# Optimization experiments

Measured on AMD Instinct MI355X. Metric: run time of the kernel, lower is better.

Reference implementation:

```python
import jax, jax.numpy as jnp
import numpy as np

F0 = 39          # FIELD_COUNT
D = 16           # embedding dim
SIZES = [128, 128, 128]  # cross_layer_sizes
B = 8192


def setup_inputs() -> dict:
    key = jax.random.key(0)
    k0, k1, k2, k3, k4 = jax.random.split(key, 5)
    nn_input = jax.random.normal(k0, (B, F0 * D), dtype=jnp.float32)
    # direct=False => field_nums: [39, 64, 64]; filters: [F0*Fk, L]
    scale = 0.02
    f0 = jax.random.normal(k1, (F0 * F0, SIZES[0]), dtype=jnp.float32) * scale
    f1 = jax.random.normal(k2, (F0 * (SIZES[0] // 2), SIZES[1]), dtype=jnp.float32) * scale
    f2 = jax.random.normal(k3, (F0 * (SIZES[1] // 2), SIZES[2]), dtype=jnp.float32) * scale
    final_len = SIZES[0] // 2 + SIZES[1] // 2 + SIZES[2]  # 256
    w_nn = jax.random.normal(k4, (final_len, 1), dtype=jnp.float32) * scale
    b_nn = jnp.zeros((1,), dtype=jnp.float32)
    return {"nn_input": nn_input, "f0": f0, "f1": f1, "f2": f2,
            "w_nn": w_nn, "b_nn": b_nn}


def reference(nn_input, f0, f1, f2, w_nn, b_nn):
    x0 = nn_input.reshape(-1, F0, D)            # [B, F0, D]
    b = x0.shape[0]
    filters = [f0, f1, f2]
    hidden = x0
    field = F0
    direct_outs = []
    n_layers = len(SIZES)
    for idx, layer_size in enumerate(SIZES):
        # dim-wise outer product: z[b,d,i*field+j] = x0[b,i,d]*hidden[b,j,d]
        z = jnp.einsum('bid,bjd->bdij', x0, hidden).reshape(b, D, F0 * field)
        if idx == 0:
            # remove self-interactions: keep strictly upper triangle, x2
            mask = jnp.triu(jnp.ones((F0, F0), dtype=z.dtype), k=1).reshape(1, 1, F0 * F0)
            z = z * mask * 2.0
        # conv1d kernel-width-1 == per-position GEMM; fuse the [0,2,1] transpose
        curr = jnp.einsum('bdc,cl->bld', z, filters[idx])   # [B, L, D]
        curr = jax.nn.relu(curr)                            # cross_activation='relu'
        if idx != n_layers - 1:
            half = layer_size // 2
            next_hidden = curr[:, :half, :]
            direct = curr[:, half:, :]
        else:
            direct = curr
            next_hidden = None
        direct_outs.append(direct)
        hidden = next_hidden
        field = layer_size // 2
    result = jnp.concatenate(direct_outs, axis=1)   # [B, final_len, D]
    rs = result.sum(axis=-1)                        # [B, final_len]
    base_score = rs.sum(axis=1, keepdims=True)      # res=True
    return base_score + rs @ w_nn + b_nn            # [B, 1]
```

## Files before the change

### kernel.cpp

```cpp
#include <hip/hip_runtime.h>


#define F0N 39
#define NB  32
#define NC16 156
#define LAYER_HALVES (NC16 * 4 * 64 * 8)

typedef _Float16 half8 __attribute__((ext_vector_type(8)));
typedef float f32x16 __attribute__((ext_vector_type(16)));

__global__ void prep_kernel(const float* __restrict__ f0,
                            const float* __restrict__ f1,
                            const float* __restrict__ f2,
                            _Float16* __restrict__ fprep) {
    int blk  = blockIdx.x;
    int l    = blk / NC16;
    int c16  = blk - l * NC16;
    int t    = threadIdx.x;
    int nt   = t >> 6;
    int lane = t & 63;
    int hf   = lane >> 5;
    int n    = nt * 32 + (lane & 31);
    const float* f = (l == 0) ? f0 : ((l == 1) ? f1 : f2);
    half8 v;
    #pragma unroll
    for (int reg = 0; reg < 8; ++reg) {
        int kg = c16 * 16 + hf * 8 + reg;
        float x;
        if (l == 0) {
            int fi = kg >> 6, fj = kg & 63;
            x = (fj < F0N) ? f[(fi * F0N + fj) * 128 + n] : 0.0f;
        } else {
            x = f[(size_t)kg * 128 + n];
        }
        v[reg] = (_Float16)x;
    }
    *(half8*)&fprep[(size_t)l * LAYER_HALVES + (((c16 * 4 + nt) * 64 + lane) << 3)] = v;
}

#define LOAD_BF(C16)                                                          \
    half8 Bf[4];                                                              \
    {                                                                         \
        _Pragma("unroll")                                                     \
        for (int nt = 0; nt < 4; ++nt)                                        \
            Bf[nt] = *(const half8*)(fpl + ((((C16) * 4 + nt) * 64 + lane) << 3)); \
    }

#define DO_MFMA()                                                             \
    {                                                                         \
        _Pragma("unroll")                                                     \
        for (int mt = 0; mt < 2; ++mt)                                        \
            _Pragma("unroll")                                                 \
            for (int nt = 0; nt < 4; ++nt)                                    \
                acc[mt][nt] = __builtin_amdgcn_mfma_f32_32x32x16_f16(         \
                    Af[mt], Bf[nt], acc[mt][nt], 0, 0, 0);                    \
    }

#define FULL_STEP(Q)                                                          \
    do {                                                                      \
        LOAD_BF(i * 4 + (Q));                                                 \
        half8 Af[2];                                                          \
        _Pragma("unroll")                                                     \
        for (int mt = 0; mt < 2; ++mt) Af[mt] = hreg[mt][(Q)] * xv2[mt];      \
        DO_MFMA();                                                            \
    } while (0)

#define PART_STEP(Q)                                                          \
    do {                                                                      \
        LOAD_BF(i * 4 + (Q));                                                 \
        const int j0 = (Q) * 16 + hf * 8;                                     \
        half8 msk;                                                            \
        _Pragma("unroll")                                                     \
        for (int reg = 0; reg < 8; ++reg)                                     \
            msk[reg] = (j0 + reg > i) ? (_Float16)1.0f : (_Float16)0.0f;      \
        half8 Af[2];                                                          \
        _Pragma("unroll")                                                     \
        for (int mt = 0; mt < 2; ++mt) Af[mt] = hreg[mt][(Q)] * (msk * xv2[mt]); \
        DO_MFMA();                                                            \
    } while (0)

__global__ __launch_bounds__(512, 2) void cin_mfma(
    const float* __restrict__ xin,
    const _Float16* __restrict__ fprep,
    const float* __restrict__ wnn,
    const float* __restrict__ bnn,
    float* __restrict__ out)
{
    __shared__ _Float16 hT[NB * 16 * 72] __attribute__((aligned(16)));
    __shared__ _Float16 xs[NB * 16 * 40] __attribute__((aligned(16)));
    __shared__ float outacc[NB];

    const int t     = threadIdx.x;
    const int wave  = t >> 6;
    const int lane  = t & 63;
    const int hf    = lane >> 5;
    const int lane5 = lane & 31;
    const int dl    = lane & 15;
    const int bt    = lane5 >> 4;
    const int wb0   = wave * 4;
    const int b0    = blockIdx.x * NB;

    for (int u = t; u < NB * 16 * 72 / 8; u += 512) ((uint4*)hT)[u] = uint4{0, 0, 0, 0};
    if (t < NB) outacc[t] = 0.0f;
    __syncthreads();

    for (int u = t; u < NB * F0N; u += 512) {
        int nb = u / F0N;
        int i  = u - nb * F0N;
        const float* src = xin + (size_t)(b0 + nb) * 624 + i * 16;
        #pragma unroll
        for (int q = 0; q < 4; ++q) {
            float4 v = *(const float4*)(src + q * 4);
            int d = q * 4;
            hT[(nb * 16 + d + 0) * 72 + i] = (_Float16)v.x;
            hT[(nb * 16 + d + 1) * 72 + i] = (_Float16)v.y;
            hT[(nb * 16 + d + 2) * 72 + i] = (_Float16)v.z;
            hT[(nb * 16 + d + 3) * 72 + i] = (_Float16)v.w;
            xs[(nb * 16 + d + 0) * 40 + i] = (_Float16)v.x;
            xs[(nb * 16 + d + 1) * 40 + i] = (_Float16)v.y;
            xs[(nb * 16 + d + 2) * 40 + i] = (_Float16)v.z;
            xs[(nb * 16 + d + 3) * 40 + i] = (_Float16)v.w;
        }
    }
    __syncthreads();

    for (int layer = 0; layer < 3; ++layer) {
        half8 hreg[2][4];
        #pragma unroll
        for (int mt = 0; mt < 2; ++mt) {
            int base = ((wb0 + mt * 2 + bt) * 16 + dl) * 72 + hf * 8;
            #pragma unroll
            for (int r = 0; r < 4; ++r)
                hreg[mt][r] = *(const half8*)&hT[base + r * 16];
        }
        __syncthreads();

        f32x16 acc[2][4];
        #pragma unroll
        for (int mt = 0; mt < 2; ++mt)
            #pragma unroll
            for (int nt = 0; nt < 4; ++nt)
                #pragma unroll
                for (int e = 0; e < 16; ++e) acc[mt][nt][e] = 0.0f;

        const _Float16* fpl = fprep + (size_t)layer * LAYER_HALVES;
        const int xrow0 = ((wb0 + bt) * 16 + dl) * 40;
        const int xrow1 = ((wb0 + 2 + bt) * 16 + dl) * 40;

        if (layer == 0) {
            _Float16 xv2[2];
            for (int i = 0; i < 16; ++i) {
                xv2[0] = (_Float16)2.0f * xs[xrow0 + i];
                xv2[1] = (_Float16)2.0f * xs[xrow1 + i];
                if (i < 15) PART_STEP(0);
                FULL_STEP(1);
                FULL_STEP(2);
            }
            for (int i = 16; i < 32; ++i) {
                xv2[0] = (_Float16)2.0f * xs[xrow0 + i];
                xv2[1] = (_Float16)2.0f * xs[xrow1 + i];
                if (i < 31) PART_STEP(1);
                FULL_STEP(2);
            }
            for (int i = 32; i < 38; ++i) {
                xv2[0] = (_Float16)2.0f * xs[xrow0 + i];
                xv2[1] = (_Float16)2.0f * xs[xrow1 + i];
                PART_STEP(2);
            }
        } else {
            _Float16 xv2[2];
            for (int i = 0; i < F0N; ++i) {
                xv2[0] = xs[xrow0 + i];
                xv2[1] = xs[xrow1 + i];
                FULL_STEP(0);
                FULL_STEP(1);
                FULL_STEP(2);
                FULL_STEP(3);
            }
        }

        const int catbase = (layer == 2) ? 128 : ((layer == 0) ? -64 : 0);
        #pragma unroll
        for (int mt = 0; mt < 2; ++mt) {
            const int nb0 = wb0 + mt * 2;
            float cm0 = 0.0f, cm1 = 0.0f;
            #pragma unroll
            for (int nt = 0; nt < 4; ++nt) {
                float r[16];
                #pragma unroll
                for (int reg = 0; reg < 16; ++reg)
                    r[reg] = fmaxf(acc[mt][nt][reg], 0.0f);
                if (layer < 2 && nt < 2) {
                    const int j = nt * 32 + lane5;
                    #pragma unroll
                    for (int reg = 0; reg < 16; ++reg) {
                        int nb = nb0 + (reg >> 3);
                        int d  = (reg & 3) + 8 * ((reg >> 2) & 1) + 4 * hf;
                        hT[(nb * 16 + d) * 72 + j] = (_Float16)r[reg];
                    }
                }
                if (layer == 2 || nt >= 2) {
                    const float w = 1.0f + wnn[catbase + nt * 32 + lane5];
                    float s0 = ((r[0] + r[1]) + (r[2] + r[3])) +
                               ((r[4] + r[5]) + (r[6] + r[7]));
                    float s1 = ((r[8] + r[9]) + (r[10] + r[11])) +
                               ((r[12] + r[13]) + (r[14] + r[15]));
                    s0 += __shfl_xor(s0, 32, 64);
                    s1 += __shfl_xor(s1, 32, 64);
                    cm0 = fmaf(s0, w, cm0);
                    cm1 = fmaf(s1, w, cm1);
                }
            }
            #pragma unroll
            for (int sh = 16; sh >= 1; sh >>= 1) {
                cm0 += __shfl_xor(cm0, sh, 64);
                cm1 += __shfl_xor(cm1, sh, 64);
            }
            if (lane == 0) {
                atomicAdd(&outacc[nb0], cm0);
                atomicAdd(&outacc[nb0 + 1], cm1);
            }
        }
        __syncthreads();
    }

    if (t < NB) out[b0 + t] = outacc[t] + bnn[0];
}

extern "C" void kernel_launch(void* const* d_in, const int* in_sizes, int n_in,
                              void* d_out, int out_size, void* d_ws, size_t ws_size,
                              hipStream_t stream) {
    const float* xin = (const float*)d_in[0];
    const float* f0g = (const float*)d_in[1];
    const float* f1g = (const float*)d_in[2];
    const float* f2g = (const float*)d_in[3];
    const float* wnn = (const float*)d_in[4];
    const float* bnn = (const float*)d_in[5];
    float* out = (float*)d_out;
    _Float16* fprep = (_Float16*)d_ws;

    prep_kernel<<<3 * NC16, 256, 0, stream>>>(f0g, f1g, f2g, fprep);

    const int B = in_sizes[0] / 624;
    cin_mfma<<<B / NB, 512, 0, stream>>>(xin, fprep, wnn, bnn, out);
}
```

Before: 255.6 us.

## Fold triangular mask into prepped filters, shrink block to 8 samples per block

The strict upper-triangle mask and the factor of 2 for layer 0 are moved into the filter prep kernel, so the inner loop no longer builds per-step masks. Each wave now handles one M-tile of two samples instead of two, halving accumulator registers. Blocks go from 512 to 256 threads over 8 samples, giving 4x more blocks and higher occupancy. The x values are stored pre-duplicated as packed half2 words so they can be splatted cheaply. The tradeoff is that each B-fragment load from global memory now feeds half as many MFMAs, which doubles filter traffic per sample.

```diff
diff --git a/kernel.cpp b/kernel.cpp
--- a/kernel.cpp
+++ b/kernel.cpp
@@ -2,9 +2,10 @@
 
 
 #define F0N 39
-#define NB  32
+#define NB  8
 #define NC16 156
 #define LAYER_HALVES (NC16 * 4 * 64 * 8)
+#define XW 41
 
 typedef _Float16 half8 __attribute__((ext_vector_type(8)));
 typedef float f32x16 __attribute__((ext_vector_type(16)));
@@ -29,7 +30,7 @@
         float x;
         if (l == 0) {
             int fi = kg >> 6, fj = kg & 63;
-            x = (fj < F0N) ? f[(fi * F0N + fj) * 128 + n] : 0.0f;
+            x = (fj < F0N && fj > fi) ? 2.0f * f[(fi * F0N + fj) * 128 + n] : 0.0f;
         } else {
             x = f[(size_t)kg * 128 + n];
         }
@@ -46,40 +47,23 @@
             Bf[nt] = *(const half8*)(fpl + ((((C16) * 4 + nt) * 64 + lane) << 3)); \
     }
 
-#define DO_MFMA()                                                             \
-    {                                                                         \
-        _Pragma("unroll")                                                     \
-        for (int mt = 0; mt < 2; ++mt)                                        \
-            _Pragma("unroll")                                                 \
-            for (int nt = 0; nt < 4; ++nt)                                    \
-                acc[mt][nt] = __builtin_amdgcn_mfma_f32_32x32x16_f16(         \
-                    Af[mt], Bf[nt], acc[mt][nt], 0, 0, 0);                    \
-    }
+static __device__ inline half8 splat8(unsigned xw) {
+    union { unsigned u[4]; half8 h; } s;
+    s.u[0] = xw; s.u[1] = xw; s.u[2] = xw; s.u[3] = xw;
+    return s.h;
+}
 
 #define FULL_STEP(Q)                                                          \
     do {                                                                      \
         LOAD_BF(i * 4 + (Q));                                                 \
-        half8 Af[2];                                                          \
+        half8 Af = hreg[(Q)] * splat8(xw);                                    \
         _Pragma("unroll")                                                     \
-        for (int mt = 0; mt < 2; ++mt) Af[mt] = hreg[mt][(Q)] * xv2[mt];      \
-        DO_MFMA();                                                            \
+        for (int nt = 0; nt < 4; ++nt)                                        \
+            acc[nt] = __builtin_amdgcn_mfma_f32_32x32x16_f16(                 \
+                Af, Bf[nt], acc[nt], 0, 0, 0);                                \
     } while (0)
 
-#define PART_STEP(Q)                                                          \
-    do {                                                                      \
-        LOAD_BF(i * 4 + (Q));                                                 \
-        const int j0 = (Q) * 16 + hf * 8;                                     \
-        half8 msk;                                                            \
-        _Pragma("unroll")                                                     \
-        for (int reg = 0; reg < 8; ++reg)                                     \
-            msk[reg] = (j0 + reg > i) ? (_Float16)1.0f : (_Float16)0.0f;      \
-        half8 Af[2];                                                          \
-        _Pragma("unroll")                                                     \
-        for (int mt = 0; mt < 2; ++mt) Af[mt] = hreg[mt][(Q)] * (msk * xv2[mt]); \
-        DO_MFMA();                                                            \
-    } while (0)
-
-__global__ __launch_bounds__(512, 2) void cin_mfma(
+__global__ __launch_bounds__(256, 4) void cin_mfma(
     const float* __restrict__ xin,
     const _Float16* __restrict__ fprep,
     const float* __restrict__ wnn,
@@ -87,7 +71,7 @@
     float* __restrict__ out)
 {
     __shared__ _Float16 hT[NB * 16 * 72] __attribute__((aligned(16)));
-    __shared__ _Float16 xs[NB * 16 * 40] __attribute__((aligned(16)));
+    __shared__ unsigned  xs2[NB * 16 * XW] __attribute__((aligned(16)));
     __shared__ float outacc[NB];
 
     const int t     = threadIdx.x;
@@ -97,14 +81,14 @@
     const int lane5 = lane & 31;
     const int dl    = lane & 15;
     const int bt    = lane5 >> 4;
-    const int wb0   = wave * 4;
+    const int nbw   = wave * 2;
     const int b0    = blockIdx.x * NB;
 
-    for (int u = t; u < NB * 16 * 72 / 8; u += 512) ((uint4*)hT)[u] = uint4{0, 0, 0, 0};
+    for (int u = t; u < NB * 16 * 72 / 8; u += 256) ((uint4*)hT)[u] = uint4{0, 0, 0, 0};
     if (t < NB) outacc[t] = 0.0f;
     __syncthreads();
 
-    for (int u = t; u < NB * F0N; u += 512) {
+    for (int u = t; u < NB * F0N; u += 256) {
         int nb = u / F0N;
         int i  = u - nb * F0N;
         const float* src = xin + (size_t)(b0 + nb) * 624 + i * 16;
@@ -112,66 +96,57 @@
         for (int q = 0; q < 4; ++q) {
             float4 v = *(const float4*)(src + q * 4);
             int d = q * 4;
+            union { _Float16 f[2]; unsigned u; } pk;
             hT[(nb * 16 + d + 0) * 72 + i] = (_Float16)v.x;
             hT[(nb * 16 + d + 1) * 72 + i] = (_Float16)v.y;
             hT[(nb * 16 + d + 2) * 72 + i] = (_Float16)v.z;
             hT[(nb * 16 + d + 3) * 72 + i] = (_Float16)v.w;
-            xs[(nb * 16 + d + 0) * 40 + i] = (_Float16)v.x;
-            xs[(nb * 16 + d + 1) * 40 + i] = (_Float16)v.y;
-            xs[(nb * 16 + d + 2) * 40 + i] = (_Float16)v.z;
-            xs[(nb * 16 + d + 3) * 40 + i] = (_Float16)v.w;
+            pk.f[0] = pk.f[1] = (_Float16)v.x; xs2[(nb * 16 + d + 0) * XW + i] = pk.u;
+            pk.f[0] = pk.f[1] = (_Float16)v.y; xs2[(nb * 16 + d + 1) * XW + i] = pk.u;
+            pk.f[0] = pk.f[1] = (_Float16)v.z; xs2[(nb * 16 + d + 2) * XW + i] = pk.u;
+            pk.f[0] = pk.f[1] = (_Float16)v.w; xs2[(nb * 16 + d + 3) * XW + i] = pk.u;
         }
     }
     __syncthreads();
 
     for (int layer = 0; layer < 3; ++layer) {
-        half8 hreg[2][4];
-        #pragma unroll
-        for (int mt = 0; mt < 2; ++mt) {
-            int base = ((wb0 + mt * 2 + bt) * 16 + dl) * 72 + hf * 8;
+        half8 hreg[4];
+        {
+            int base = ((nbw + bt) * 16 + dl) * 72 + hf * 8;
             #pragma unroll
             for (int r = 0; r < 4; ++r)
-                hreg[mt][r] = *(const half8*)&hT[base + r * 16];
+                hreg[r] = *(const half8*)&hT[base + r * 16];
         }
         __syncthreads();
 
-        f32x16 acc[2][4];
-        #pragma unroll
-        for (int mt = 0; mt < 2; ++mt)
+        f32x16 acc[4];
+        #pragma unroll
+        for (int nt = 0; nt < 4; ++nt)
             #pragma unroll
-            for (int nt = 0; nt < 4; ++nt)
-                #pragma unroll
-                for (int e = 0; e < 16; ++e) acc[mt][nt][e] = 0.0f;
+            for (int e = 0; e < 16; ++e) acc[nt][e] = 0.0f;
 
         const _Float16* fpl = fprep + (size_t)layer * LAYER_HALVES;
-        const int xrow0 = ((wb0 + bt) * 16 + dl) * 40;
-        const int xrow1 = ((wb0 + 2 + bt) * 16 + dl) * 40;
+        const int xrow = ((nbw + bt) * 16 + dl) * XW;
 
         if (layer == 0) {
-            _Float16 xv2[2];
             for (int i = 0; i < 16; ++i) {
-                xv2[0] = (_Float16)2.0f * xs[xrow0 + i];
-                xv2[1] = (_Float16)2.0f * xs[xrow1 + i];
-                if (i < 15) PART_STEP(0);
+                const unsigned xw = xs2[xrow + i];
+                if (i < 15) FULL_STEP(0);
                 FULL_STEP(1);
                 FULL_STEP(2);
             }
             for (int i = 16; i < 32; ++i) {
-                xv2[0] = (_Float16)2.0f * xs[xrow0 + i];
-                xv2[1] = (_Float16)2.0f * xs[xrow1 + i];
-                if (i < 31) PART_STEP(1);
+                const unsigned xw = xs2[xrow + i];
+                if (i < 31) FULL_STEP(1);
                 FULL_STEP(2);
             }
             for (int i = 32; i < 38; ++i) {
-                xv2[0] = (_Float16)2.0f * xs[xrow0 + i];
-                xv2[1] = (_Float16)2.0f * xs[xrow1 + i];
-                PART_STEP(2);
+                const unsigned xw = xs2[xrow + i];
+                FULL_STEP(2);
             }
         } else {
-            _Float16 xv2[2];
             for (int i = 0; i < F0N; ++i) {
-                xv2[0] = xs[xrow0 + i];
-                xv2[1] = xs[xrow1 + i];
+                const unsigned xw = xs2[xrow + i];
                 FULL_STEP(0);
                 FULL_STEP(1);
                 FULL_STEP(2);
@@ -180,46 +155,42 @@
         }
 
         const int catbase = (layer == 2) ? 128 : ((layer == 0) ? -64 : 0);
-        #pragma unroll
-        for (int mt = 0; mt < 2; ++mt) {
-            const int nb0 = wb0 + mt * 2;
-            float cm0 = 0.0f, cm1 = 0.0f;
+        float cm0 = 0.0f, cm1 = 0.0f;
+        #pragma unroll
+        for (int nt = 0; nt < 4; ++nt) {
+            float r[16];
             #pragma unroll
-            for (int nt = 0; nt < 4; ++nt) {
-                float r[16];
+            for (int reg = 0; reg < 16; ++reg)
+                r[reg] = fmaxf(acc[nt][reg], 0.0f);
+            if (layer < 2 && nt < 2) {
+                const int j = nt * 32 + lane5;
                 #pragma unroll
-                for (int reg = 0; reg < 16; ++reg)
-                    r[reg] = fmaxf(acc[mt][nt][reg], 0.0f);
-                if (layer < 2 && nt < 2) {
-                    const int j = nt * 32 + lane5;
-                    #pragma unroll
-                    for (int reg = 0; reg < 16; ++reg) {
-                        int nb = nb0 + (reg >> 3);
-                        int d  = (reg & 3) + 8 * ((reg >> 2) & 1) + 4 * hf;
-                        hT[(nb * 16 + d) * 72 + j] = (_Float16)r[reg];
-                    }
+                for (int reg = 0; reg < 16; ++reg) {
+                    int nb = nbw + (reg >> 3);
+                    int d  = (reg & 3) + 8 * ((reg >> 2) & 1) + 4 * hf;
+                    hT[(nb * 16 + d) * 72 + j] = (_Float16)r[reg];
                 }
-                if (layer == 2 || nt >= 2) {
-                    const float w = 1.0f + wnn[catbase + nt * 32 + lane5];
-                    float s0 = ((r[0] + r[1]) + (r[2] + r[3])) +
-                               ((r[4] + r[5]) + (r[6] + r[7]));
-                    float s1 = ((r[8] + r[9]) + (r[10] + r[11])) +
-                               ((r[12] + r[13]) + (r[14] + r[15]));
-                    s0 += __shfl_xor(s0, 32, 64);
-                    s1 += __shfl_xor(s1, 32, 64);
-                    cm0 = fmaf(s0, w, cm0);
-                    cm1 = fmaf(s1, w, cm1);
-                }
-            }
-            #pragma unroll
-            for (int sh = 16; sh >= 1; sh >>= 1) {
-                cm0 += __shfl_xor(cm0, sh, 64);
-                cm1 += __shfl_xor(cm1, sh, 64);
-            }
-            if (lane == 0) {
-                atomicAdd(&outacc[nb0], cm0);
-                atomicAdd(&outacc[nb0 + 1], cm1);
-            }
+            }
+            if (layer == 2 || nt >= 2) {
+                const float w = 1.0f + wnn[catbase + nt * 32 + lane5];
+                float s0 = ((r[0] + r[1]) + (r[2] + r[3])) +
+                           ((r[4] + r[5]) + (r[6] + r[7]));
+                float s1 = ((r[8] + r[9]) + (r[10] + r[11])) +
+                           ((r[12] + r[13]) + (r[14] + r[15]));
+                s0 += __shfl_xor(s0, 32, 64);
+                s1 += __shfl_xor(s1, 32, 64);
+                cm0 = fmaf(s0, w, cm0);
+                cm1 = fmaf(s1, w, cm1);
+            }
+        }
+        #pragma unroll
+        for (int sh = 16; sh >= 1; sh >>= 1) {
+            cm0 += __shfl_xor(cm0, sh, 64);
+            cm1 += __shfl_xor(cm1, sh, 64);
+        }
+        if (lane == 0) {
+            atomicAdd(&outacc[nbw], cm0);
+            atomicAdd(&outacc[nbw + 1], cm1);
         }
         __syncthreads();
     }
@@ -242,5 +213,5 @@
     prep_kernel<<<3 * NC16, 256, 0, stream>>>(f0g, f1g, f2g, fprep);
 
     const int B = in_sizes[0] / 624;
-    cin_mfma<<<B / NB, 512, 0, stream>>>(xin, fprep, wnn, bnn, out);
-}
+    cin_mfma<<<B / NB, 256, 0, stream>>>(xin, fprep, wnn, bnn, out);
+}
```

Measured after the change: 603.0 us. 2.36x slower.

## Stage filter tiles through double-buffered LDS and fold triangle mask into weights

Applied to the files above, without the earlier changes.

Filter fragments were previously loaded straight from global memory by every wave. Now the block cooperatively loads each per-i filter slice into a double-buffered shared-memory stage, prefetching the next slice while MFMAs run on the current one. The layer-0 upper-triangle mask and the factor of 2 are moved into the prepared filter weights, so the per-step mask construction goes away. The cost is 32 KB of extra LDS, which may reduce occupancy, plus a block-wide barrier on every iteration.

```diff
diff --git a/kernel.cpp b/kernel.cpp
--- a/kernel.cpp
+++ b/kernel.cpp
@@ -5,6 +5,7 @@
 #define NB  32
 #define NC16 156
 #define LAYER_HALVES (NC16 * 4 * 64 * 8)
+#define IHALFS 8192
 
 typedef _Float16 half8 __attribute__((ext_vector_type(8)));
 typedef float f32x16 __attribute__((ext_vector_type(16)));
@@ -29,7 +30,7 @@
         float x;
         if (l == 0) {
             int fi = kg >> 6, fj = kg & 63;
-            x = (fj < F0N) ? f[(fi * F0N + fj) * 128 + n] : 0.0f;
+            x = (fj < F0N && fj > fi) ? 2.0f * f[(fi * F0N + fj) * 128 + n] : 0.0f;
         } else {
             x = f[(size_t)kg * 128 + n];
         }
@@ -38,45 +39,34 @@
     *(half8*)&fprep[(size_t)l * LAYER_HALVES + (((c16 * 4 + nt) * 64 + lane) << 3)] = v;
 }
 
-#define LOAD_BF(C16)                                                          \
-    half8 Bf[4];                                                              \
-    {                                                                         \
+#define FULL_STEP_LS(Q)                                                       \
+    do {                                                                      \
+        half8 Bf[4];                                                          \
         _Pragma("unroll")                                                     \
         for (int nt = 0; nt < 4; ++nt)                                        \
-            Bf[nt] = *(const half8*)(fpl + ((((C16) * 4 + nt) * 64 + lane) << 3)); \
-    }
-
-#define DO_MFMA()                                                             \
-    {                                                                         \
+            Bf[nt] = *(const half8*)&bcur[(((Q) * 4 + nt) * 64 + lane) << 3]; \
+        half8 Af[2];                                                          \
+        _Pragma("unroll")                                                     \
+        for (int mt = 0; mt < 2; ++mt) Af[mt] = hreg[mt][(Q)] * xv2[mt];      \
         _Pragma("unroll")                                                     \
         for (int mt = 0; mt < 2; ++mt)                                        \
             _Pragma("unroll")                                                 \
             for (int nt = 0; nt < 4; ++nt)                                    \
                 acc[mt][nt] = __builtin_amdgcn_mfma_f32_32x32x16_f16(         \
                     Af[mt], Bf[nt], acc[mt][nt], 0, 0, 0);                    \
-    }
-
-#define FULL_STEP(Q)                                                          \
+    } while (0)
+
+#define STAGE_LOAD(IP)                                                        \
     do {                                                                      \
-        LOAD_BF(i * 4 + (Q));                                                 \
-        half8 Af[2];                                                          \
-        _Pragma("unroll")                                                     \
-        for (int mt = 0; mt < 2; ++mt) Af[mt] = hreg[mt][(Q)] * xv2[mt];      \
-        DO_MFMA();                                                            \
+        const uint4* g = (const uint4*)(fpl + (size_t)(IP) * IHALFS);         \
+        s0 = g[t];                                                            \
+        s1 = g[t + 512];                                                      \
     } while (0)
 
-#define PART_STEP(Q)                                                          \
+#define STAGE_WRITE(BUFP)                                                     \
     do {                                                                      \
-        LOAD_BF(i * 4 + (Q));                                                 \
-        const int j0 = (Q) * 16 + hf * 8;                                     \
-        half8 msk;                                                            \
-        _Pragma("unroll")                                                     \
-        for (int reg = 0; reg < 8; ++reg)                                     \
-            msk[reg] = (j0 + reg > i) ? (_Float16)1.0f : (_Float16)0.0f;      \
-        half8 Af[2];                                                          \
-        _Pragma("unroll")                                                     \
-        for (int mt = 0; mt < 2; ++mt) Af[mt] = hreg[mt][(Q)] * (msk * xv2[mt]); \
-        DO_MFMA();                                                            \
+        ((uint4*)(BUFP))[t]       = s0;                                       \
+        ((uint4*)(BUFP))[t + 512] = s1;                                       \
     } while (0)
 
 __global__ __launch_bounds__(512, 2) void cin_mfma(
@@ -88,6 +78,7 @@
 {
     __shared__ _Float16 hT[NB * 16 * 72] __attribute__((aligned(16)));
     __shared__ _Float16 xs[NB * 16 * 40] __attribute__((aligned(16)));
+    __shared__ _Float16 bst[2][IHALFS] __attribute__((aligned(16)));
     __shared__ float outacc[NB];
 
     const int t     = threadIdx.x;
@@ -125,6 +116,11 @@
     __syncthreads();
 
     for (int layer = 0; layer < 3; ++layer) {
+        const _Float16* fpl = fprep + (size_t)layer * LAYER_HALVES;
+        uint4 s0, s1;
+
+        STAGE_LOAD(0);
+
         half8 hreg[2][4];
         #pragma unroll
         for (int mt = 0; mt < 2; ++mt) {
@@ -133,6 +129,9 @@
             for (int r = 0; r < 4; ++r)
                 hreg[mt][r] = *(const half8*)&hT[base + r * 16];
         }
+        __syncthreads();
+
+        STAGE_WRITE(bst[0]);
         __syncthreads();
 
         f32x16 acc[2][4];
@@ -143,39 +142,37 @@
                 #pragma unroll
                 for (int e = 0; e < 16; ++e) acc[mt][nt][e] = 0.0f;
 
-        const _Float16* fpl = fprep + (size_t)layer * LAYER_HALVES;
         const int xrow0 = ((wb0 + bt) * 16 + dl) * 40;
         const int xrow1 = ((wb0 + 2 + bt) * 16 + dl) * 40;
 
         if (layer == 0) {
             _Float16 xv2[2];
-            for (int i = 0; i < 16; ++i) {
-                xv2[0] = (_Float16)2.0f * xs[xrow0 + i];
-                xv2[1] = (_Float16)2.0f * xs[xrow1 + i];
-                if (i < 15) PART_STEP(0);
-                FULL_STEP(1);
-                FULL_STEP(2);
-            }
-            for (int i = 16; i < 32; ++i) {
-                xv2[0] = (_Float16)2.0f * xs[xrow0 + i];
-                xv2[1] = (_Float16)2.0f * xs[xrow1 + i];
-                if (i < 31) PART_STEP(1);
-                FULL_STEP(2);
-            }
-            for (int i = 32; i < 38; ++i) {
-                xv2[0] = (_Float16)2.0f * xs[xrow0 + i];
-                xv2[1] = (_Float16)2.0f * xs[xrow1 + i];
-                PART_STEP(2);
+            for (int i = 0; i < 38; ++i) {
+                const _Float16* bcur = bst[i & 1];
+                _Float16* bnxt = bst[(i & 1) ^ 1];
+                if (i < 37) STAGE_LOAD(i + 1);
+                xv2[0] = xs[xrow0 + i];
+                xv2[1] = xs[xrow1 + i];
+                if (i < 15) FULL_STEP_LS(0);
+                if (i < 31) FULL_STEP_LS(1);
+                if (i < 37) STAGE_WRITE(bnxt);
+                FULL_STEP_LS(2);
+                __syncthreads();
             }
         } else {
             _Float16 xv2[2];
             for (int i = 0; i < F0N; ++i) {
+                const _Float16* bcur = bst[i & 1];
+                _Float16* bnxt = bst[(i & 1) ^ 1];
+                if (i < F0N - 1) STAGE_LOAD(i + 1);
                 xv2[0] = xs[xrow0 + i];
                 xv2[1] = xs[xrow1 + i];
-                FULL_STEP(0);
-                FULL_STEP(1);
-                FULL_STEP(2);
-                FULL_STEP(3);
+                FULL_STEP_LS(0);
+                FULL_STEP_LS(1);
+                FULL_STEP_LS(2);
+                if (i < F0N - 1) STAGE_WRITE(bnxt);
+                FULL_STEP_LS(3);
+                __syncthreads();
             }
         }
 
@@ -201,14 +198,14 @@
                 }
                 if (layer == 2 || nt >= 2) {
                     const float w = 1.0f + wnn[catbase + nt * 32 + lane5];
-                    float s0 = ((r[0] + r[1]) + (r[2] + r[3])) +
-                               ((r[4] + r[5]) + (r[6] + r[7]));
-                    float s1 = ((r[8] + r[9]) + (r[10] + r[11])) +
-                               ((r[12] + r[13]) + (r[14] + r[15]));
-                    s0 += __shfl_xor(s0, 32, 64);
-                    s1 += __shfl_xor(s1, 32, 64);
-                    cm0 = fmaf(s0, w, cm0);
-                    cm1 = fmaf(s1, w, cm1);
+                    float s0r = ((r[0] + r[1]) + (r[2] + r[3])) +
+                                ((r[4] + r[5]) + (r[6] + r[7]));
+                    float s1r = ((r[8] + r[9]) + (r[10] + r[11])) +
+                                ((r[12] + r[13]) + (r[14] + r[15]));
+                    s0r += __shfl_xor(s0r, 32, 64);
+                    s1r += __shfl_xor(s1r, 32, 64);
+                    cm0 = fmaf(s0r, w, cm0);
+                    cm1 = fmaf(s1r, w, cm1);
                 }
             }
             #pragma unroll
```

New measurement: 238.1 us, median of 2. 6.8% less time.
